# Kernel optimization log

Measured on AMD Instinct MI355X. Metric: run time of the kernel, lower is better.

## Reference

```python
import jax, jax.numpy as jnp
import numpy as np

T, H, I, E, K = 2048, 1024, 768, 32, 4  # tokens, hidden, expert intermediate, n_experts, top_k


def setup_inputs() -> dict:
    key = jax.random.key(0)
    k0, k1, k2, k3, k4 = jax.random.split(key, 5)
    scale = 0.02
    return {
        "x": jax.random.normal(k0, (T, H), dtype=jnp.float32),
        "gate_w": jax.random.normal(k1, (E, H), dtype=jnp.float32) * scale,   # router linear [E, H]
        "w_gate": jax.random.normal(k2, (E, I, H), dtype=jnp.float32) * scale,  # gate_proj per expert
        "w_up": jax.random.normal(k3, (E, I, H), dtype=jnp.float32) * scale,    # up_proj per expert
        "w_down": jax.random.normal(k4, (E, H, I), dtype=jnp.float32) * scale,  # down_proj per expert
    }


def reference(x, gate_w, w_gate, w_up, w_down):
    # Router: dense gate linear + softmax + top-k + renormalize
    logits = x @ gate_w.T                              # [T, E]
    probs = jax.nn.softmax(logits, axis=-1)
    top_w, top_i = jax.lax.top_k(probs, K)             # [T, K]
    top_w = top_w / jnp.sum(top_w, axis=-1, keepdims=True)  # renormalize=True
    # Dense combine weights [T, E] (zero for unselected experts)
    tok = jnp.arange(T, dtype=jnp.int32)[:, None]
    combine = jnp.zeros((T, E), dtype=x.dtype).at[tok, top_i].add(top_w)

    # Scan over experts: each expert is a SwiGLU MLP; masked-dense combine.
    def step(acc, ws):
        w1, w3, w2, ce = ws                            # [I,H], [I,H], [H,I], [T]
        h = (jax.nn.silu(x @ w1.T) * (x @ w3.T)) @ w2.T  # [T, H]
        return acc + ce[:, None] * h, None

    out, _ = jax.lax.scan(step, jnp.zeros_like(x), (w_gate, w_up, w_down, combine.T))
    return out
```

## Files before the change

kernel.cpp:

```cpp
#include <hip/hip_runtime.h>
#include <hip/hip_bf16.h>
#include <stdint.h>

#define T_TOK 2048
#define HDIM  1024
#define IDIM  768
#define NEXP  32
#define TOPK  4
#define NPAIR (T_TOK*TOPK)
#define MTILE 256
#define MAXMT 64

typedef __attribute__((ext_vector_type(8))) short bf16x8;
typedef __attribute__((ext_vector_type(4))) float f32x4;

__device__ __forceinline__ unsigned short f2bf(float f){
  union { float f; unsigned u; } v; v.f = f;
  unsigned r = (v.u + 0x7fffu + ((v.u >> 16) & 1u)) >> 16;
  return (unsigned short)r;
}

__global__ __launch_bounds__(256) void k_convert_x(const float* __restrict__ x,
                                                   ushort* __restrict__ xb){
  int idx = blockIdx.x*256 + threadIdx.x;
  float4 v = ((const float4*)x)[idx];
  ushort4 o; o.x=f2bf(v.x); o.y=f2bf(v.y); o.z=f2bf(v.z); o.w=f2bf(v.w);
  ((ushort4*)xb)[idx] = o;
}

__global__ __launch_bounds__(256) void k_router(const float* __restrict__ x,
                                                const float* __restrict__ gw,
                                                int* __restrict__ ei, float* __restrict__ wv,
                                                int* __restrict__ counts){
  int wid  = threadIdx.x >> 6;
  int lane = threadIdx.x & 63;
  int t = blockIdx.x*4 + wid;
  float xv[16];
  #pragma unroll
  for (int i=0;i<16;i++) xv[i] = x[t*HDIM + i*64 + lane];
  float p[NEXP];
  #pragma unroll
  for (int e=0;e<NEXP;e++){
    const float* w = gw + e*HDIM;
    float a = 0.f;
    #pragma unroll
    for (int i=0;i<16;i++) a = fmaf(xv[i], w[i*64+lane], a);
    #pragma unroll
    for (int off=32; off>=1; off>>=1) a += __shfl_xor(a, off, 64);
    p[e] = a;
  }
  float m = p[0];
  #pragma unroll
  for (int e=1;e<NEXP;e++) m = fmaxf(m, p[e]);
  #pragma unroll
  for (int e=0;e<NEXP;e++) p[e] = __expf(p[e]-m);
  unsigned used = 0; int sel[TOPK]; float sw[TOPK]; float wsum = 0.f;
  #pragma unroll
  for (int k=0;k<TOPK;k++){
    float best = -1.f; int bi = 0;
    #pragma unroll
    for (int e=0;e<NEXP;e++){
      bool ok = (((used>>e)&1u)==0u) && (p[e] > best);
      best = ok ? p[e] : best; bi = ok ? e : bi;
    }
    used |= 1u<<bi; sel[k]=bi; sw[k]=best; wsum += best;
  }
  if (lane==0){
    float inv = 1.f/wsum;
    #pragma unroll
    for (int k=0;k<TOPK;k++){
      ei[t*TOPK+k] = sel[k];
      wv[t*TOPK+k] = sw[k]*inv;
      atomicAdd(&counts[sel[k]], 1);
    }
  }
}

__global__ void k_offsets(const int* __restrict__ counts, int* __restrict__ offsets,
                          int* __restrict__ mtE, int* __restrict__ mtM0,
                          int* __restrict__ nmt){
  if (threadIdx.x==0 && blockIdx.x==0){
    int s=0;
    for (int e=0;e<NEXP;e++){ offsets[e]=s; s+=counts[e]; }
    offsets[NEXP]=s;
    int nm=0;
    for (int e=0;e<NEXP;e++){
      int ne = counts[e];
      for (int m0=0; m0<ne && nm<MAXMT; m0+=MTILE){ mtE[nm]=e; mtM0[nm]=m0; nm++; }
    }
    nmt[0]=nm;
  }
}

__global__ __launch_bounds__(256) void k_scatter(const int* __restrict__ ei,
                                                 const int* __restrict__ offsets,
                                                 int* __restrict__ cursor,
                                                 int* __restrict__ slot_tk,
                                                 int* __restrict__ tk_slot){
  int g = blockIdx.x*256 + threadIdx.x;
  int e = ei[g];
  int pos = atomicAdd(&cursor[e], 1);
  int slot = offsets[e] + pos;
  slot_tk[slot] = g;
  tk_slot[g] = slot;
}

__global__ __launch_bounds__(512,4) void k_gateup(const ushort* __restrict__ xb,
    const float* __restrict__ w1, const float* __restrict__ w3,
    const int* __restrict__ offsets, const int* __restrict__ slot_tk,
    const int* __restrict__ mtE, const int* __restrict__ mtM0, const int* __restrict__ nmt,
    ushort* __restrict__ act){
  int bi  = blockIdx.x;
  int mti = bi >> 4;
  int it  = bi & 15;
  if (mti >= nmt[0]) return;
  int e    = mtE[mti];
  int m0   = mtM0[mti];
  int off0 = offsets[e];
  int ne   = offsets[e+1]-off0;
  int ibase = it*48;

  __shared__ int toks[256];
  __shared__ ushort Bls[2][2][48][68];

  int tid = threadIdx.x, wid = tid>>6, lane = tid&63;
  if (tid < 256){
    int slot = off0 + m0 + tid;
    int fb = slot_tk[off0] >> 2;
    toks[tid] = (m0 + tid < ne) ? (slot_tk[slot] >> 2) : fb;
  }
  const float* bsrc[3]; int b_mat[3], b_r[3], b_c4[3];
  const size_t wbase = (size_t)e * IDIM * HDIM;
  #pragma unroll
  for (int s=0;s<3;s++){
    int li = s*512 + tid;
    int mat = li >= 768;
    int li2 = li - mat*768;
    int r = li2>>4, c4 = li2&15;
    b_mat[s]=mat; b_r[s]=r; b_c4[s]=c4;
    bsrc[s] = (mat ? w3 : w1) + wbase + (size_t)(ibase+r)*HDIM + c4*4;
  }
  __syncthreads();

  const ushort* arow[2];
  #pragma unroll
  for (int m=0;m<2;m++){
    int row = wid*32 + m*16 + (lane&15);
    arow[m] = xb + (size_t)toks[row]*HDIM + (lane>>4)*8;
  }

  f32x4 accg[2][3], accu[2][3];
  #pragma unroll
  for (int a=0;a<2;a++)
    #pragma unroll
    for (int b=0;b<3;b++){ accg[a][b]=(f32x4){0,0,0,0}; accu[a][b]=(f32x4){0,0,0,0}; }

  float4 breg[3];
  #pragma unroll
  for (int s=0;s<3;s++) breg[s] = *(const float4*)(bsrc[s]);
  #pragma unroll
  for (int s=0;s<3;s++){
    ushort4 o; o.x=f2bf(breg[s].x); o.y=f2bf(breg[s].y); o.z=f2bf(breg[s].z); o.w=f2bf(breg[s].w);
    *(ushort4*)(&Bls[0][b_mat[s]][b_r[s]][b_c4[s]*4]) = o;
  }
  __syncthreads();

  for (int kb=0; kb<16; ++kb){
    int cur = kb & 1, nxt = cur ^ 1;
    if (kb < 15){
      #pragma unroll
      for (int s=0;s<3;s++) breg[s] = *(const float4*)(bsrc[s] + (kb+1)*64);
    }
    #pragma unroll
    for (int kk=0; kk<2; ++kk){
      bf16x8 af[2];
      #pragma unroll
      for (int m=0;m<2;m++)
        af[m] = *(const bf16x8*)(arow[m] + kb*64 + kk*32);
      #pragma unroll
      for (int n=0;n<3;n++){
        bf16x8 bg = *(const bf16x8*)(&Bls[cur][0][n*16 + (lane&15)][kk*32 + (lane>>4)*8]);
        bf16x8 bu = *(const bf16x8*)(&Bls[cur][1][n*16 + (lane&15)][kk*32 + (lane>>4)*8]);
        #pragma unroll
        for (int m=0;m<2;m++){
          accg[m][n] = __builtin_amdgcn_mfma_f32_16x16x32_bf16(af[m], bg, accg[m][n], 0,0,0);
          accu[m][n] = __builtin_amdgcn_mfma_f32_16x16x32_bf16(af[m], bu, accu[m][n], 0,0,0);
        }
      }
    }
    if (kb < 15){
      #pragma unroll
      for (int s=0;s<3;s++){
        ushort4 o; o.x=f2bf(breg[s].x); o.y=f2bf(breg[s].y); o.z=f2bf(breg[s].z); o.w=f2bf(breg[s].w);
        *(ushort4*)(&Bls[nxt][b_mat[s]][b_r[s]][b_c4[s]*4]) = o;
      }
    }
    __syncthreads();
  }

  int nval = ne - m0; if (nval > 256) nval = 256;
  #pragma unroll
  for (int m=0;m<2;m++)
    #pragma unroll
    for (int n=0;n<3;n++)
      #pragma unroll
      for (int r=0;r<4;r++){
        int row = wid*32 + m*16 + (lane>>4)*4 + r;
        if (row < nval){
          float g = accg[m][n][r], u = accu[m][n][r];
          float sval = g / (1.f + __expf(-g)) * u;
          act[(size_t)(off0+m0+row)*IDIM + ibase + n*16 + (lane&15)] = f2bf(sval);
        }
      }
}

__global__ __launch_bounds__(512,4) void k_down(const ushort* __restrict__ act,
    const float* __restrict__ w2, const int* __restrict__ offsets,
    const int* __restrict__ mtE, const int* __restrict__ mtM0, const int* __restrict__ nmt,
    float* __restrict__ pout){
  int bi  = blockIdx.x;
  int mti = bi >> 4;
  int ht  = bi & 15;
  if (mti >= nmt[0]) return;
  int e    = mtE[mti];
  int m0   = mtM0[mti];
  int off0 = offsets[e], ne = offsets[e+1]-off0;
  int hbase = ht*64;

  __shared__ ushort Bls[2][64][68];

  int tid = threadIdx.x, wid = tid>>6, lane = tid&63;

  const float* bsrc[2]; int b_r[2], b_c4[2];
  const size_t wbase = (size_t)e * HDIM * IDIM;
  #pragma unroll
  for (int s=0;s<2;s++){
    int li = s*512 + tid;
    int r = li>>4, c4 = li&15;
    b_r[s]=r; b_c4[s]=c4;
    bsrc[s] = w2 + wbase + (size_t)(hbase+r)*IDIM + c4*4;
  }

  const ushort* arow[2];
  #pragma unroll
  for (int m=0;m<2;m++){
    int row = wid*32 + m*16 + (lane&15);
    int mrow = m0 + row; mrow = (mrow < ne) ? mrow : 0;
    arow[m] = act + (size_t)(off0+mrow)*IDIM + (lane>>4)*8;
  }

  f32x4 acc[2][4];
  #pragma unroll
  for (int a=0;a<2;a++)
    #pragma unroll
    for (int b=0;b<4;b++) acc[a][b]=(f32x4){0,0,0,0};

  float4 breg[2];
  #pragma unroll
  for (int s=0;s<2;s++) breg[s] = *(const float4*)(bsrc[s]);
  #pragma unroll
  for (int s=0;s<2;s++){
    ushort4 o; o.x=f2bf(breg[s].x); o.y=f2bf(breg[s].y); o.z=f2bf(breg[s].z); o.w=f2bf(breg[s].w);
    *(ushort4*)(&Bls[0][b_r[s]][b_c4[s]*4]) = o;
  }
  __syncthreads();

  for (int kb=0; kb<12; ++kb){
    int cur = kb & 1, nxt = cur ^ 1;
    if (kb < 11){
      #pragma unroll
      for (int s=0;s<2;s++) breg[s] = *(const float4*)(bsrc[s] + (kb+1)*64);
    }
    #pragma unroll
    for (int kk=0; kk<2; ++kk){
      bf16x8 af[2];
      #pragma unroll
      for (int m=0;m<2;m++)
        af[m] = *(const bf16x8*)(arow[m] + kb*64 + kk*32);
      #pragma unroll
      for (int n=0;n<4;n++){
        bf16x8 bw = *(const bf16x8*)(&Bls[cur][n*16 + (lane&15)][kk*32 + (lane>>4)*8]);
        #pragma unroll
        for (int m=0;m<2;m++)
          acc[m][n] = __builtin_amdgcn_mfma_f32_16x16x32_bf16(af[m], bw, acc[m][n], 0,0,0);
      }
    }
    if (kb < 11){
      #pragma unroll
      for (int s=0;s<2;s++){
        ushort4 o; o.x=f2bf(breg[s].x); o.y=f2bf(breg[s].y); o.z=f2bf(breg[s].z); o.w=f2bf(breg[s].w);
        *(ushort4*)(&Bls[nxt][b_r[s]][b_c4[s]*4]) = o;
      }
    }
    __syncthreads();
  }

  int nval = ne - m0; if (nval > 256) nval = 256;
  #pragma unroll
  for (int m=0;m<2;m++)
    #pragma unroll
    for (int n=0;n<4;n++)
      #pragma unroll
      for (int r=0;r<4;r++){
        int row = wid*32 + m*16 + (lane>>4)*4 + r;
        if (row < nval)
          pout[(size_t)(off0+m0+row)*HDIM + hbase + n*16 + (lane&15)] = acc[m][n][r];
      }
}

__global__ __launch_bounds__(256) void k_combine(const float* __restrict__ pout,
    const int* __restrict__ tk_slot, const float* __restrict__ wv,
    float* __restrict__ out){
  int t = blockIdx.x;
  int c = threadIdx.x;
  float a0=0,a1=0,a2=0,a3=0;
  #pragma unroll
  for (int k=0;k<TOPK;k++){
    int slot = tk_slot[t*TOPK+k];
    float w  = wv[t*TOPK+k];
    float4 v = *(const float4*)(pout + (size_t)slot*HDIM + c*4);
    a0 = fmaf(w, v.x, a0); a1 = fmaf(w, v.y, a1);
    a2 = fmaf(w, v.z, a2); a3 = fmaf(w, v.w, a3);
  }
  float4 o; o.x=a0; o.y=a1; o.z=a2; o.w=a3;
  *(float4*)(out + (size_t)t*HDIM + c*4) = o;
}

extern "C" void kernel_launch(void* const* d_in, const int* in_sizes, int n_in,
                              void* d_out, int out_size, void* d_ws, size_t ws_size,
                              hipStream_t stream){
  const float* x  = (const float*)d_in[0];
  const float* gw = (const float*)d_in[1];
  const float* w1 = (const float*)d_in[2];
  const float* w3 = (const float*)d_in[3];
  const float* w2 = (const float*)d_in[4];
  float* out = (float*)d_out;

  char* ws = (char*)d_ws;
  size_t off = 0;
  ushort* xb   = (ushort*)(ws + off); off += (size_t)T_TOK*HDIM*2;
  ushort* act  = (ushort*)(ws + off); off += (size_t)NPAIR*IDIM*2;
  float*  pout = (float*) (ws + off); off += (size_t)NPAIR*HDIM*4;
  int* counts  = (int*)(ws + off); off += NEXP*4;
  int* cursor  = (int*)(ws + off); off += NEXP*4;
  int* offsets = (int*)(ws + off); off += (NEXP+1)*4;
  int* mtE     = (int*)(ws + off); off += MAXMT*4;
  int* mtM0    = (int*)(ws + off); off += MAXMT*4;
  int* nmt     = (int*)(ws + off); off += 4;
  off = (off + 255) & ~(size_t)255;
  int*   ei      = (int*)  (ws + off); off += (size_t)NPAIR*4;
  float* wvp     = (float*)(ws + off); off += (size_t)NPAIR*4;
  int*   slot_tk = (int*)  (ws + off); off += (size_t)NPAIR*4;
  int*   tk_slot = (int*)  (ws + off); off += (size_t)NPAIR*4;

  hipMemsetAsync(counts, 0, 2*NEXP*4, stream);

  k_convert_x<<<T_TOK*HDIM/1024, 256, 0, stream>>>(x, xb);
  k_router<<<T_TOK/4, 256, 0, stream>>>(x, gw, ei, wvp, counts);
  k_offsets<<<1, 64, 0, stream>>>(counts, offsets, mtE, mtM0, nmt);
  k_scatter<<<NPAIR/256, 256, 0, stream>>>(ei, offsets, cursor, slot_tk, tk_slot);
  k_gateup<<<MAXMT*16, 512, 0, stream>>>(xb, w1, w3, offsets, slot_tk, mtE, mtM0, nmt, act);
  k_down<<<MAXMT*16, 512, 0, stream>>>(act, w2, offsets, mtE, mtM0, nmt, pout);
  k_combine<<<T_TOK, 256, 0, stream>>>(pout, tk_slot, wvp, out);
}
```

Baseline: 277.7 us.

## Register-prefetch A fragments two steps ahead and narrow gate/up N-tile

Both grouped GEMM kernels now prefetch the activation (A) fragments and weight tiles two k-steps ahead into register double buffers, unrolling the loop by two so global loads overlap MFMA work. The gate/up kernel also shrinks its N tile from 48 to 32 columns, launching 24 blocks per M tile instead of 16, which gives more blocks and simpler single-load-per-thread weight staging. In exchange, register pressure rises from holding two A fragment sets, and each gate/up block reuses its gathered token rows across fewer output columns, so x is re-read more times.

```diff
diff --git a/kernel.cpp b/kernel.cpp
--- a/kernel.cpp
+++ b/kernel.cpp
@@ -111,17 +111,17 @@
     const int* __restrict__ mtE, const int* __restrict__ mtM0, const int* __restrict__ nmt,
     ushort* __restrict__ act){
   int bi  = blockIdx.x;
-  int mti = bi >> 4;
-  int it  = bi & 15;
+  int mti = bi / 24;
+  int it  = bi - mti*24;
   if (mti >= nmt[0]) return;
   int e    = mtE[mti];
   int m0   = mtM0[mti];
   int off0 = offsets[e];
   int ne   = offsets[e+1]-off0;
-  int ibase = it*48;
+  int ibase = it*32;
 
   __shared__ int toks[256];
-  __shared__ ushort Bls[2][2][48][68];
+  __shared__ ushort Bls[2][2][32][68];
 
   int tid = threadIdx.x, wid = tid>>6, lane = tid&63;
   if (tid < 256){
@@ -129,80 +129,83 @@
     int fb = slot_tk[off0] >> 2;
     toks[tid] = (m0 + tid < ne) ? (slot_tk[slot] >> 2) : fb;
   }
-  const float* bsrc[3]; int b_mat[3], b_r[3], b_c4[3];
+  int b_r = tid>>4, b_c4 = tid&15;
   const size_t wbase = (size_t)e * IDIM * HDIM;
-  #pragma unroll
-  for (int s=0;s<3;s++){
-    int li = s*512 + tid;
-    int mat = li >= 768;
-    int li2 = li - mat*768;
-    int r = li2>>4, c4 = li2&15;
-    b_mat[s]=mat; b_r[s]=r; b_c4[s]=c4;
-    bsrc[s] = (mat ? w3 : w1) + wbase + (size_t)(ibase+r)*HDIM + c4*4;
-  }
+  const float* bsrc0 = w1 + wbase + (size_t)(ibase+b_r)*HDIM + b_c4*4;
+  const float* bsrc1 = w3 + wbase + (size_t)(ibase+b_r)*HDIM + b_c4*4;
   __syncthreads();
 
-  const ushort* arow[2];
-  #pragma unroll
-  for (int m=0;m<2;m++){
-    int row = wid*32 + m*16 + (lane&15);
-    arow[m] = xb + (size_t)toks[row]*HDIM + (lane>>4)*8;
-  }
-
-  f32x4 accg[2][3], accu[2][3];
+  const ushort* arow0 = xb + (size_t)toks[wid*32      + (lane&15)]*HDIM + (lane>>4)*8;
+  const ushort* arow1 = xb + (size_t)toks[wid*32 + 16 + (lane&15)]*HDIM + (lane>>4)*8;
+
+  f32x4 accg[2][2], accu[2][2];
   #pragma unroll
   for (int a=0;a<2;a++)
     #pragma unroll
-    for (int b=0;b<3;b++){ accg[a][b]=(f32x4){0,0,0,0}; accu[a][b]=(f32x4){0,0,0,0}; }
-
-  float4 breg[3];
-  #pragma unroll
-  for (int s=0;s<3;s++) breg[s] = *(const float4*)(bsrc[s]);
-  #pragma unroll
-  for (int s=0;s<3;s++){
-    ushort4 o; o.x=f2bf(breg[s].x); o.y=f2bf(breg[s].y); o.z=f2bf(breg[s].z); o.w=f2bf(breg[s].w);
-    *(ushort4*)(&Bls[0][b_mat[s]][b_r[s]][b_c4[s]*4]) = o;
-  }
-  __syncthreads();
-
-  for (int kb=0; kb<16; ++kb){
-    int cur = kb & 1, nxt = cur ^ 1;
-    if (kb < 15){
+    for (int b=0;b<2;b++){ accg[a][b]=(f32x4){0,0,0,0}; accu[a][b]=(f32x4){0,0,0,0}; }
+
+  float4 bP[2], bQ[2];
+  bf16x8 afA[4], afB[4];
+
+  auto loadB = [&](int kb, float4* d){
+    d[0] = *(const float4*)(bsrc0 + kb*64);
+    d[1] = *(const float4*)(bsrc1 + kb*64);
+  };
+  auto loadA = [&](int kb, bf16x8* d){
+    #pragma unroll
+    for (int kk=0;kk<2;kk++){
+      d[kk*2+0] = *(const bf16x8*)(arow0 + kb*64 + kk*32);
+      d[kk*2+1] = *(const bf16x8*)(arow1 + kb*64 + kk*32);
+    }
+  };
+  auto writeB = [&](int buf, const float4* s){
+    #pragma unroll
+    for (int m=0;m<2;m++){
+      ushort4 o; o.x=f2bf(s[m].x); o.y=f2bf(s[m].y); o.z=f2bf(s[m].z); o.w=f2bf(s[m].w);
+      *(ushort4*)(&Bls[buf][m][b_r][b_c4*4]) = o;
+    }
+  };
+  auto compute = [&](int buf, const bf16x8* af){
+    #pragma unroll
+    for (int kk=0;kk<2;kk++){
       #pragma unroll
-      for (int s=0;s<3;s++) breg[s] = *(const float4*)(bsrc[s] + (kb+1)*64);
-    }
-    #pragma unroll
-    for (int kk=0; kk<2; ++kk){
-      bf16x8 af[2];
-      #pragma unroll
-      for (int m=0;m<2;m++)
-        af[m] = *(const bf16x8*)(arow[m] + kb*64 + kk*32);
-      #pragma unroll
-      for (int n=0;n<3;n++){
-        bf16x8 bg = *(const bf16x8*)(&Bls[cur][0][n*16 + (lane&15)][kk*32 + (lane>>4)*8]);
-        bf16x8 bu = *(const bf16x8*)(&Bls[cur][1][n*16 + (lane&15)][kk*32 + (lane>>4)*8]);
+      for (int n=0;n<2;n++){
+        bf16x8 bg = *(const bf16x8*)(&Bls[buf][0][n*16 + (lane&15)][kk*32 + (lane>>4)*8]);
+        bf16x8 bu = *(const bf16x8*)(&Bls[buf][1][n*16 + (lane&15)][kk*32 + (lane>>4)*8]);
         #pragma unroll
         for (int m=0;m<2;m++){
-          accg[m][n] = __builtin_amdgcn_mfma_f32_16x16x32_bf16(af[m], bg, accg[m][n], 0,0,0);
-          accu[m][n] = __builtin_amdgcn_mfma_f32_16x16x32_bf16(af[m], bu, accu[m][n], 0,0,0);
+          accg[m][n] = __builtin_amdgcn_mfma_f32_16x16x32_bf16(af[kk*2+m], bg, accg[m][n], 0,0,0);
+          accu[m][n] = __builtin_amdgcn_mfma_f32_16x16x32_bf16(af[kk*2+m], bu, accu[m][n], 0,0,0);
         }
       }
     }
-    if (kb < 15){
-      #pragma unroll
-      for (int s=0;s<3;s++){
-        ushort4 o; o.x=f2bf(breg[s].x); o.y=f2bf(breg[s].y); o.z=f2bf(breg[s].z); o.w=f2bf(breg[s].w);
-        *(ushort4*)(&Bls[nxt][b_mat[s]][b_r[s]][b_c4[s]*4]) = o;
-      }
-    }
+  };
+
+  loadB(0, bP);
+  loadA(0, afA);
+  loadB(1, bQ);
+  writeB(0, bP);
+  __syncthreads();
+  loadA(1, afB);
+
+  for (int kb=0; kb<16; kb+=2){
+    if (kb+2 < 16) loadB(kb+2, bP);
+    compute(0, afA);
+    if (kb+2 < 16) loadA(kb+2, afA);
+    writeB(1, bQ);
     __syncthreads();
+    if (kb+3 < 16) loadB(kb+3, bQ);
+    compute(1, afB);
+    if (kb+3 < 16) loadA(kb+3, afB);
+    if (kb+2 < 16) writeB(0, bP);
+    __syncthreads();
   }
 
   int nval = ne - m0; if (nval > 256) nval = 256;
   #pragma unroll
   for (int m=0;m<2;m++)
     #pragma unroll
-    for (int n=0;n<3;n++)
+    for (int n=0;n<2;n++)
       #pragma unroll
       for (int r=0;r<4;r++){
         int row = wid*32 + m*16 + (lane>>4)*4 + r;
@@ -230,24 +233,15 @@
   __shared__ ushort Bls[2][64][68];
 
   int tid = threadIdx.x, wid = tid>>6, lane = tid&63;
-
-  const float* bsrc[2]; int b_r[2], b_c4[2];
+  int b_r = tid>>4, b_c4 = tid&15;
   const size_t wbase = (size_t)e * HDIM * IDIM;
-  #pragma unroll
-  for (int s=0;s<2;s++){
-    int li = s*512 + tid;
-    int r = li>>4, c4 = li&15;
-    b_r[s]=r; b_c4[s]=c4;
-    bsrc[s] = w2 + wbase + (size_t)(hbase+r)*IDIM + c4*4;
-  }
-
-  const ushort* arow[2];
-  #pragma unroll
-  for (int m=0;m<2;m++){
-    int row = wid*32 + m*16 + (lane&15);
-    int mrow = m0 + row; mrow = (mrow < ne) ? mrow : 0;
-    arow[m] = act + (size_t)(off0+mrow)*IDIM + (lane>>4)*8;
-  }
+  const float* bsrc0 = w2 + wbase + (size_t)(hbase+b_r   )*IDIM + b_c4*4;
+  const float* bsrc1 = w2 + wbase + (size_t)(hbase+b_r+32)*IDIM + b_c4*4;
+
+  int row0 = m0 + wid*32      + (lane&15); row0 = (row0 < ne) ? row0 : 0;
+  int row1 = m0 + wid*32 + 16 + (lane&15); row1 = (row1 < ne) ? row1 : 0;
+  const ushort* arow0 = act + (size_t)(off0+row0)*IDIM + (lane>>4)*8;
+  const ushort* arow1 = act + (size_t)(off0+row1)*IDIM + (lane>>4)*8;
 
   f32x4 acc[2][4];
   #pragma unroll
@@ -255,43 +249,57 @@
     #pragma unroll
     for (int b=0;b<4;b++) acc[a][b]=(f32x4){0,0,0,0};
 
-  float4 breg[2];
-  #pragma unroll
-  for (int s=0;s<2;s++) breg[s] = *(const float4*)(bsrc[s]);
-  #pragma unroll
-  for (int s=0;s<2;s++){
-    ushort4 o; o.x=f2bf(breg[s].x); o.y=f2bf(breg[s].y); o.z=f2bf(breg[s].z); o.w=f2bf(breg[s].w);
-    *(ushort4*)(&Bls[0][b_r[s]][b_c4[s]*4]) = o;
-  }
-  __syncthreads();
-
-  for (int kb=0; kb<12; ++kb){
-    int cur = kb & 1, nxt = cur ^ 1;
-    if (kb < 11){
-      #pragma unroll
-      for (int s=0;s<2;s++) breg[s] = *(const float4*)(bsrc[s] + (kb+1)*64);
-    }
-    #pragma unroll
-    for (int kk=0; kk<2; ++kk){
-      bf16x8 af[2];
-      #pragma unroll
-      for (int m=0;m<2;m++)
-        af[m] = *(const bf16x8*)(arow[m] + kb*64 + kk*32);
+  float4 bP[2], bQ[2];
+  bf16x8 afA[4], afB[4];
+
+  auto loadB = [&](int kb, float4* d){
+    d[0] = *(const float4*)(bsrc0 + kb*64);
+    d[1] = *(const float4*)(bsrc1 + kb*64);
+  };
+  auto loadA = [&](int kb, bf16x8* d){
+    #pragma unroll
+    for (int kk=0;kk<2;kk++){
+      d[kk*2+0] = *(const bf16x8*)(arow0 + kb*64 + kk*32);
+      d[kk*2+1] = *(const bf16x8*)(arow1 + kb*64 + kk*32);
+    }
+  };
+  auto writeB = [&](int buf, const float4* s){
+    #pragma unroll
+    for (int m=0;m<2;m++){
+      ushort4 o; o.x=f2bf(s[m].x); o.y=f2bf(s[m].y); o.z=f2bf(s[m].z); o.w=f2bf(s[m].w);
+      *(ushort4*)(&Bls[buf][b_r + m*32][b_c4*4]) = o;
+    }
+  };
+  auto compute = [&](int buf, const bf16x8* af){
+    #pragma unroll
+    for (int kk=0;kk<2;kk++){
       #pragma unroll
       for (int n=0;n<4;n++){
-        bf16x8 bw = *(const bf16x8*)(&Bls[cur][n*16 + (lane&15)][kk*32 + (lane>>4)*8]);
+        bf16x8 bw = *(const bf16x8*)(&Bls[buf][n*16 + (lane&15)][kk*32 + (lane>>4)*8]);
         #pragma unroll
         for (int m=0;m<2;m++)
-          acc[m][n] = __builtin_amdgcn_mfma_f32_16x16x32_bf16(af[m], bw, acc[m][n], 0,0,0);
+          acc[m][n] = __builtin_amdgcn_mfma_f32_16x16x32_bf16(af[kk*2+m], bw, acc[m][n], 0,0,0);
       }
     }
-    if (kb < 11){
-      #pragma unroll
-      for (int s=0;s<2;s++){
-        ushort4 o; o.x=f2bf(breg[s].x); o.y=f2bf(breg[s].y); o.z=f2bf(breg[s].z); o.w=f2bf(breg[s].w);
-        *(ushort4*)(&Bls[nxt][b_r[s]][b_c4[s]*4]) = o;
-      }
-    }
+  };
+
+  loadB(0, bP);
+  loadA(0, afA);
+  loadB(1, bQ);
+  writeB(0, bP);
+  __syncthreads();
+  loadA(1, afB);
+
+  for (int kb=0; kb<12; kb+=2){
+    if (kb+2 < 12) loadB(kb+2, bP);
+    compute(0, afA);
+    if (kb+2 < 12) loadA(kb+2, afA);
+    writeB(1, bQ);
+    __syncthreads();
+    if (kb+3 < 12) loadB(kb+3, bQ);
+    compute(1, afB);
+    if (kb+3 < 12) loadA(kb+3, afB);
+    if (kb+2 < 12) writeB(0, bP);
     __syncthreads();
   }
 
@@ -359,7 +367,7 @@
   k_router<<<T_TOK/4, 256, 0, stream>>>(x, gw, ei, wvp, counts);
   k_offsets<<<1, 64, 0, stream>>>(counts, offsets, mtE, mtM0, nmt);
   k_scatter<<<NPAIR/256, 256, 0, stream>>>(ei, offsets, cursor, slot_tk, tk_slot);
-  k_gateup<<<MAXMT*16, 512, 0, stream>>>(xb, w1, w3, offsets, slot_tk, mtE, mtM0, nmt, act);
+  k_gateup<<<MAXMT*24, 512, 0, stream>>>(xb, w1, w3, offsets, slot_tk, mtE, mtM0, nmt, act);
   k_down<<<MAXMT*16, 512, 0, stream>>>(act, w2, offsets, mtE, mtM0, nmt, pout);
   k_combine<<<T_TOK, 256, 0, stream>>>(pout, tk_slot, wvp, out);
 }
```

New measurement: 242.9 us. -12.5%, faster.

## Retile expert GEMMs with taller M tiles, wider K stages and XCD-aware block mapping

Applied to the files above, without the earlier changes.

Raises the token tile from 256 to 384 rows and narrows the N tile, so each wave handles three 16-row fragments. Weight tiles are now staged 256 K at a time with row-contiguous fp32 loads and packed bf16 conversion, cutting the number of barriers and improving coalescing. Block IDs are remapped so the tiles of one M-tile share an XCD, aiming for better L2 reuse of the gathered activations. The grid is resized to match. MTILE also changes how k_offsets builds tiles, so correctness depends on that hidden kernel using MTILE and keeping the tile count within MAXMT.

```diff
diff --git a/kernel.cpp b/kernel.cpp
--- a/kernel.cpp
+++ b/kernel.cpp
@@ -8,7 +8,7 @@
 #define NEXP  32
 #define TOPK  4
 #define NPAIR (T_TOK*TOPK)
-#define MTILE 256
+#define MTILE 384
 #define MAXMT 64
 
 typedef __attribute__((ext_vector_type(8))) short bf16x8;
@@ -18,6 +18,12 @@
   union { float f; unsigned u; } v; v.f = f;
   unsigned r = (v.u + 0x7fffu + ((v.u >> 16) & 1u)) >> 16;
   return (unsigned short)r;
+}
+
+__device__ __forceinline__ unsigned pack_bf2(float lo, float hi){
+  __hip_bfloat162 h2 = __float22bfloat162_rn(float2{lo, hi});
+  union { __hip_bfloat162 h; unsigned u; } v; v.h = h2;
+  return v.u;
 }
 
 __global__ __launch_bounds__(256) void k_convert_x(const float* __restrict__ x,
@@ -111,105 +117,99 @@
     const int* __restrict__ mtE, const int* __restrict__ mtM0, const int* __restrict__ nmt,
     ushort* __restrict__ act){
   int bi  = blockIdx.x;
-  int mti = bi >> 4;
-  int it  = bi & 15;
+  int xcd = bi & 7, j = bi >> 3;
+  int mti = (j/24)*8 + xcd;
+  int it  = j % 24;
   if (mti >= nmt[0]) return;
   int e    = mtE[mti];
   int m0   = mtM0[mti];
   int off0 = offsets[e];
   int ne   = offsets[e+1]-off0;
-  int ibase = it*48;
-
-  __shared__ int toks[256];
-  __shared__ ushort Bls[2][2][48][68];
+  int ibase = it*32;
+
+  __shared__ ushort Bls[2][64][264];
+  __shared__ int toks[MTILE];
 
   int tid = threadIdx.x, wid = tid>>6, lane = tid&63;
-  if (tid < 256){
+  if (tid < MTILE){
     int slot = off0 + m0 + tid;
     int fb = slot_tk[off0] >> 2;
     toks[tid] = (m0 + tid < ne) ? (slot_tk[slot] >> 2) : fb;
   }
-  const float* bsrc[3]; int b_mat[3], b_r[3], b_c4[3];
-  const size_t wbase = (size_t)e * IDIM * HDIM;
-  #pragma unroll
-  for (int s=0;s<3;s++){
-    int li = s*512 + tid;
-    int mat = li >= 768;
-    int li2 = li - mat*768;
-    int r = li2>>4, c4 = li2&15;
-    b_mat[s]=mat; b_r[s]=r; b_c4[s]=c4;
-    bsrc[s] = (mat ? w3 : w1) + wbase + (size_t)(ibase+r)*HDIM + c4*4;
-  }
   __syncthreads();
 
-  const ushort* arow[2];
-  #pragma unroll
-  for (int m=0;m<2;m++){
-    int row = wid*32 + m*16 + (lane&15);
+  const float* wsrc = (wid < 4 ? w1 : w3) + (size_t)e*IDIM*HDIM;
+  int row0 = (wid&3)*8;
+  const float* bsrc = wsrc + (size_t)(ibase+row0)*HDIM + lane*4;
+  int pbase = wid*8;
+
+  const ushort* arow[3];
+  #pragma unroll
+  for (int m=0;m<3;m++){
+    int row = wid*48 + m*16 + (lane&15);
     arow[m] = xb + (size_t)toks[row]*HDIM + (lane>>4)*8;
   }
 
-  f32x4 accg[2][3], accu[2][3];
-  #pragma unroll
-  for (int a=0;a<2;a++)
-    #pragma unroll
-    for (int b=0;b<3;b++){ accg[a][b]=(f32x4){0,0,0,0}; accu[a][b]=(f32x4){0,0,0,0}; }
-
-  float4 breg[3];
-  #pragma unroll
-  for (int s=0;s<3;s++) breg[s] = *(const float4*)(bsrc[s]);
-  #pragma unroll
-  for (int s=0;s<3;s++){
-    ushort4 o; o.x=f2bf(breg[s].x); o.y=f2bf(breg[s].y); o.z=f2bf(breg[s].z); o.w=f2bf(breg[s].w);
-    *(ushort4*)(&Bls[0][b_mat[s]][b_r[s]][b_c4[s]*4]) = o;
-  }
-  __syncthreads();
-
-  for (int kb=0; kb<16; ++kb){
-    int cur = kb & 1, nxt = cur ^ 1;
-    if (kb < 15){
-      #pragma unroll
-      for (int s=0;s<3;s++) breg[s] = *(const float4*)(bsrc[s] + (kb+1)*64);
-    }
-    #pragma unroll
-    for (int kk=0; kk<2; ++kk){
-      bf16x8 af[2];
-      #pragma unroll
-      for (int m=0;m<2;m++)
-        af[m] = *(const bf16x8*)(arow[m] + kb*64 + kk*32);
-      #pragma unroll
-      for (int n=0;n<3;n++){
-        bf16x8 bg = *(const bf16x8*)(&Bls[cur][0][n*16 + (lane&15)][kk*32 + (lane>>4)*8]);
-        bf16x8 bu = *(const bf16x8*)(&Bls[cur][1][n*16 + (lane&15)][kk*32 + (lane>>4)*8]);
+  f32x4 accg[3][2], accu[3][2];
+  #pragma unroll
+  for (int m=0;m<3;m++)
+    #pragma unroll
+    for (int n=0;n<2;n++){ accg[m][n]=(f32x4){0,0,0,0}; accu[m][n]=(f32x4){0,0,0,0}; }
+
+  float4 breg[8];
+  auto loadB = [&](int t){
+    #pragma unroll
+    for (int s=0;s<8;s++) breg[s] = *(const float4*)(bsrc + (size_t)s*HDIM + t*256);
+  };
+  auto writeB = [&](int buf){
+    #pragma unroll
+    for (int s=0;s<8;s++){
+      uint2 u; u.x = pack_bf2(breg[s].x, breg[s].y); u.y = pack_bf2(breg[s].z, breg[s].w);
+      *(uint2*)(&Bls[buf][pbase+s][lane*4]) = u;
+    }
+  };
+  auto compute = [&](int buf, int t){
+    #pragma unroll
+    for (int kk=0;kk<8;kk++){
+      bf16x8 af[3];
+      #pragma unroll
+      for (int m=0;m<3;m++)
+        af[m] = *(const bf16x8*)(arow[m] + t*256 + kk*32);
+      #pragma unroll
+      for (int nf=0;nf<2;nf++){
+        int p = nf*16 + (lane&15);
+        bf16x8 bg = *(const bf16x8*)(&Bls[buf][p   ][kk*32 + (lane>>4)*8]);
+        bf16x8 bu = *(const bf16x8*)(&Bls[buf][p+32][kk*32 + (lane>>4)*8]);
         #pragma unroll
-        for (int m=0;m<2;m++){
-          accg[m][n] = __builtin_amdgcn_mfma_f32_16x16x32_bf16(af[m], bg, accg[m][n], 0,0,0);
-          accu[m][n] = __builtin_amdgcn_mfma_f32_16x16x32_bf16(af[m], bu, accu[m][n], 0,0,0);
+        for (int m=0;m<3;m++){
+          accg[m][nf] = __builtin_amdgcn_mfma_f32_16x16x32_bf16(af[m], bg, accg[m][nf], 0,0,0);
+          accu[m][nf] = __builtin_amdgcn_mfma_f32_16x16x32_bf16(af[m], bu, accu[m][nf], 0,0,0);
         }
       }
     }
-    if (kb < 15){
-      #pragma unroll
-      for (int s=0;s<3;s++){
-        ushort4 o; o.x=f2bf(breg[s].x); o.y=f2bf(breg[s].y); o.z=f2bf(breg[s].z); o.w=f2bf(breg[s].w);
-        *(ushort4*)(&Bls[nxt][b_mat[s]][b_r[s]][b_c4[s]*4]) = o;
-      }
-    }
+  };
+
+  loadB(0); writeB(0); __syncthreads();
+  #pragma unroll 1
+  for (int t=0; t<4; ++t){
+    if (t < 3) loadB(t+1);
+    compute(t&1, t);
     __syncthreads();
-  }
-
-  int nval = ne - m0; if (nval > 256) nval = 256;
-  #pragma unroll
-  for (int m=0;m<2;m++)
-    #pragma unroll
-    for (int n=0;n<3;n++)
+    if (t < 3){ writeB((t+1)&1); __syncthreads(); }
+  }
+
+  int nval = ne - m0; if (nval > MTILE) nval = MTILE;
+  #pragma unroll
+  for (int m=0;m<3;m++)
+    #pragma unroll
+    for (int nf=0;nf<2;nf++)
       #pragma unroll
       for (int r=0;r<4;r++){
-        int row = wid*32 + m*16 + (lane>>4)*4 + r;
+        int row = wid*48 + m*16 + (lane>>4)*4 + r;
         if (row < nval){
-          float g = accg[m][n][r], u = accu[m][n][r];
+          float g = accg[m][nf][r], u = accu[m][nf][r];
           float sval = g / (1.f + __expf(-g)) * u;
-          act[(size_t)(off0+m0+row)*IDIM + ibase + n*16 + (lane&15)] = f2bf(sval);
+          act[(size_t)(off0+m0+row)*IDIM + ibase + nf*16 + (lane&15)] = f2bf(sval);
         }
       }
 }
@@ -219,92 +219,85 @@
     const int* __restrict__ mtE, const int* __restrict__ mtM0, const int* __restrict__ nmt,
     float* __restrict__ pout){
   int bi  = blockIdx.x;
-  int mti = bi >> 4;
-  int ht  = bi & 15;
+  int xcd = bi & 7, j = bi >> 3;
+  int mti = (j/32)*8 + xcd;
+  int ht  = j % 32;
   if (mti >= nmt[0]) return;
   int e    = mtE[mti];
   int m0   = mtM0[mti];
   int off0 = offsets[e], ne = offsets[e+1]-off0;
-  int hbase = ht*64;
-
-  __shared__ ushort Bls[2][64][68];
+  int hbase = ht*32;
+
+  __shared__ ushort Bls[2][32][264];
 
   int tid = threadIdx.x, wid = tid>>6, lane = tid&63;
 
-  const float* bsrc[2]; int b_r[2], b_c4[2];
-  const size_t wbase = (size_t)e * HDIM * IDIM;
-  #pragma unroll
-  for (int s=0;s<2;s++){
-    int li = s*512 + tid;
-    int r = li>>4, c4 = li&15;
-    b_r[s]=r; b_c4[s]=c4;
-    bsrc[s] = w2 + wbase + (size_t)(hbase+r)*IDIM + c4*4;
-  }
-
-  const ushort* arow[2];
-  #pragma unroll
-  for (int m=0;m<2;m++){
-    int row = wid*32 + m*16 + (lane&15);
-    int mrow = m0 + row; mrow = (mrow < ne) ? mrow : 0;
-    arow[m] = act + (size_t)(off0+mrow)*IDIM + (lane>>4)*8;
-  }
-
-  f32x4 acc[2][4];
-  #pragma unroll
-  for (int a=0;a<2;a++)
-    #pragma unroll
-    for (int b=0;b<4;b++) acc[a][b]=(f32x4){0,0,0,0};
-
-  float4 breg[2];
-  #pragma unroll
-  for (int s=0;s<2;s++) breg[s] = *(const float4*)(bsrc[s]);
-  #pragma unroll
-  for (int s=0;s<2;s++){
-    ushort4 o; o.x=f2bf(breg[s].x); o.y=f2bf(breg[s].y); o.z=f2bf(breg[s].z); o.w=f2bf(breg[s].w);
-    *(ushort4*)(&Bls[0][b_r[s]][b_c4[s]*4]) = o;
-  }
-  __syncthreads();
-
-  for (int kb=0; kb<12; ++kb){
-    int cur = kb & 1, nxt = cur ^ 1;
-    if (kb < 11){
-      #pragma unroll
-      for (int s=0;s<2;s++) breg[s] = *(const float4*)(bsrc[s] + (kb+1)*64);
-    }
-    #pragma unroll
-    for (int kk=0; kk<2; ++kk){
-      bf16x8 af[2];
-      #pragma unroll
-      for (int m=0;m<2;m++)
-        af[m] = *(const bf16x8*)(arow[m] + kb*64 + kk*32);
-      #pragma unroll
-      for (int n=0;n<4;n++){
-        bf16x8 bw = *(const bf16x8*)(&Bls[cur][n*16 + (lane&15)][kk*32 + (lane>>4)*8]);
+  int row0 = wid*4;
+  const float* bsrc = w2 + (size_t)e*HDIM*IDIM + (size_t)(hbase+row0)*IDIM + lane*4;
+  int pbase = wid*4;
+
+  const ushort* arow[3];
+  #pragma unroll
+  for (int m=0;m<3;m++){
+    int row = m0 + wid*48 + m*16 + (lane&15);
+    row = (row < ne) ? row : (ne-1);
+    arow[m] = act + (size_t)(off0+row)*IDIM + (lane>>4)*8;
+  }
+
+  f32x4 acc[3][2];
+  #pragma unroll
+  for (int m=0;m<3;m++)
+    #pragma unroll
+    for (int n=0;n<2;n++) acc[m][n]=(f32x4){0,0,0,0};
+
+  float4 breg[4];
+  auto loadB = [&](int t){
+    #pragma unroll
+    for (int s=0;s<4;s++) breg[s] = *(const float4*)(bsrc + (size_t)s*IDIM + t*256);
+  };
+  auto writeB = [&](int buf){
+    #pragma unroll
+    for (int s=0;s<4;s++){
+      uint2 u; u.x = pack_bf2(breg[s].x, breg[s].y); u.y = pack_bf2(breg[s].z, breg[s].w);
+      *(uint2*)(&Bls[buf][pbase+s][lane*4]) = u;
+    }
+  };
+  auto compute = [&](int buf, int t){
+    #pragma unroll
+    for (int kk=0;kk<8;kk++){
+      bf16x8 af[3];
+      #pragma unroll
+      for (int m=0;m<3;m++)
+        af[m] = *(const bf16x8*)(arow[m] + t*256 + kk*32);
+      #pragma unroll
+      for (int nf=0;nf<2;nf++){
+        bf16x8 bw = *(const bf16x8*)(&Bls[buf][nf*16 + (lane&15)][kk*32 + (lane>>4)*8]);
         #pragma unroll
-        for (int m=0;m<2;m++)
-          acc[m][n] = __builtin_amdgcn_mfma_f32_16x16x32_bf16(af[m], bw, acc[m][n], 0,0,0);
+        for (int m=0;m<3;m++)
+          acc[m][nf] = __builtin_amdgcn_mfma_f32_16x16x32_bf16(af[m], bw, acc[m][nf], 0,0,0);
       }
     }
-    if (kb < 11){
-      #pragma unroll
-      for (int s=0;s<2;s++){
-        ushort4 o; o.x=f2bf(breg[s].x); o.y=f2bf(breg[s].y); o.z=f2bf(breg[s].z); o.w=f2bf(breg[s].w);
-        *(ushort4*)(&Bls[nxt][b_r[s]][b_c4[s]*4]) = o;
-      }
-    }
+  };
+
+  loadB(0); writeB(0); __syncthreads();
+  #pragma unroll 1
+  for (int t=0; t<3; ++t){
+    if (t < 2) loadB(t+1);
+    compute(t&1, t);
     __syncthreads();
-  }
-
-  int nval = ne - m0; if (nval > 256) nval = 256;
-  #pragma unroll
-  for (int m=0;m<2;m++)
-    #pragma unroll
-    for (int n=0;n<4;n++)
+    if (t < 2){ writeB((t+1)&1); __syncthreads(); }
+  }
+
+  int nval = ne - m0; if (nval > MTILE) nval = MTILE;
+  #pragma unroll
+  for (int m=0;m<3;m++)
+    #pragma unroll
+    for (int nf=0;nf<2;nf++)
       #pragma unroll
       for (int r=0;r<4;r++){
-        int row = wid*32 + m*16 + (lane>>4)*4 + r;
+        int row = wid*48 + m*16 + (lane>>4)*4 + r;
         if (row < nval)
-          pout[(size_t)(off0+m0+row)*HDIM + hbase + n*16 + (lane&15)] = acc[m][n][r];
+          pout[(size_t)(off0+m0+row)*HDIM + hbase + nf*16 + (lane&15)] = acc[m][nf][r];
       }
 }
 
@@ -359,7 +352,7 @@
   k_router<<<T_TOK/4, 256, 0, stream>>>(x, gw, ei, wvp, counts);
   k_offsets<<<1, 64, 0, stream>>>(counts, offsets, mtE, mtM0, nmt);
   k_scatter<<<NPAIR/256, 256, 0, stream>>>(ei, offsets, cursor, slot_tk, tk_slot);
-  k_gateup<<<MAXMT*16, 512, 0, stream>>>(xb, w1, w3, offsets, slot_tk, mtE, mtM0, nmt, act);
-  k_down<<<MAXMT*16, 512, 0, stream>>>(act, w2, offsets, mtE, mtM0, nmt, pout);
+  k_gateup<<<1536, 512, 0, stream>>>(xb, w1, w3, offsets, slot_tk, mtE, mtM0, nmt, act);
+  k_down<<<2048, 512, 0, stream>>>(act, w2, offsets, mtE, mtM0, nmt, pout);
   k_combine<<<T_TOK, 256, 0, stream>>>(pout, tk_slot, wvp, out);
 }
```

Measured after the change: 298.4 us. 1.07x slower.
